# Performance work log

Measured on AMD Instinct MI355X. Metric: run time of the kernel, lower is better.

Reference implementation:

```python
import jax, jax.numpy as jnp
import numpy as np
from jax import lax

DN = ('NCHW', 'OIHW', 'NCHW')


def conv3x3(x, w, b):
    return lax.conv_general_dilated(x, w, (1, 1), 'SAME', dimension_numbers=DN) + b[None, :, None, None]


def conv1x1(x, w, b):
    # w: [O, I] -> pointwise conv
    return jnp.einsum('oi,bihw->bohw', w, x) + b[None, :, None, None]


def sft(x0, x1, sc0w, sc0b, sc1w, sc1b, sh0w, sh0b, sh1w, sh1b):
    scale = conv1x1(jax.nn.leaky_relu(conv1x1(x1, sc0w, sc0b), 0.1), sc1w, sc1b)
    shift = conv1x1(jax.nn.leaky_relu(conv1x1(x1, sh0w, sh0b), 0.1), sh1w, sh1b)
    return x0 * (scale + 1.0) + shift


def deform_conv(x, offset, w, b):
    # torchvision DeformConv2d, 3x3, stride 1, pad 1, dilation 1, no mask.
    B, C, H, W = x.shape
    O = w.shape[0]
    K = 9
    off = offset.reshape(B, K, 2, H, W)  # (dy, dx) per kernel tap
    ki = jnp.arange(3, dtype=x.dtype) - 1.0
    ky = jnp.repeat(ki, 3)  # [9]
    kx = jnp.tile(ki, 3)
    hh = jnp.arange(H, dtype=x.dtype)
    ww = jnp.arange(W, dtype=x.dtype)
    py = off[:, :, 0] + hh[None, None, :, None] + ky[None, :, None, None]  # [B,K,H,W]
    px = off[:, :, 1] + ww[None, None, None, :] + kx[None, :, None, None]
    y0f = jnp.floor(py)
    x0f = jnp.floor(px)
    wy = (py - y0f)[:, None]  # [B,1,K,H,W]
    wx = (px - x0f)[:, None]
    y0 = y0f.astype(jnp.int32)
    x0i = x0f.astype(jnp.int32)
    x_flat = x.reshape(B, C, H * W)

    def gather(iy, ix):
        valid = (iy >= 0) & (iy < H) & (ix >= 0) & (ix < W)
        idx = (jnp.clip(iy, 0, H - 1) * W + jnp.clip(ix, 0, W - 1)).reshape(B, K * H * W)
        vals = jax.vmap(lambda xf, ii: xf[:, ii])(x_flat, idx)  # [B,C,K*H*W]
        return vals.reshape(B, C, K, H, W) * valid[:, None].astype(x.dtype)

    v00 = gather(y0, x0i)
    v01 = gather(y0, x0i + 1)
    v10 = gather(y0 + 1, x0i)
    v11 = gather(y0 + 1, x0i + 1)
    samp = (v00 * (1 - wy) * (1 - wx) + v01 * (1 - wy) * wx
            + v10 * wy * (1 - wx) + v11 * wy * wx)  # [B,C,K,H,W]
    return jnp.einsum('bckhw,ock->bohw', samp, w.reshape(O, C, K)) + b[None, :, None, None]


def setup_inputs() -> dict:
    key = jax.random.key(0)
    ks = jax.random.split(key, 32)
    B, C0, C1, H, W = 4, 128, 32, 96, 96
    f32 = jnp.float32
    d = {
        'x0': jax.random.normal(ks[0], (B, C0, H, W), f32),
        'x1': jax.random.normal(ks[1], (B, C1, H, W), f32),
        'w_off': jax.random.normal(ks[2], (18, C0, 3, 3), f32) * 0.02,
        'b_off': jnp.zeros((18,), f32),
        's1_sc0_w': jax.random.normal(ks[3], (C0, C1), f32) * 0.05,
        's1_sc0_b': jnp.zeros((C0,), f32),
        's1_sc1_w': jax.random.normal(ks[4], (C0, C0), f32) * 0.05,
        's1_sc1_b': jnp.zeros((C0,), f32),
        's1_sh0_w': jax.random.normal(ks[5], (C0, C1), f32) * 0.05,
        's1_sh0_b': jnp.zeros((C0,), f32),
        's1_sh1_w': jax.random.normal(ks[6], (C0, C0), f32) * 0.05,
        's1_sh1_b': jnp.zeros((C0,), f32),
        'w_d1': jax.random.normal(ks[7], (C0, C0, 3, 3), f32) * 0.03,
        'b_d1': jnp.zeros((C0,), f32),
        's2_sc0_w': jax.random.normal(ks[8], (C0, C1), f32) * 0.05,
        's2_sc0_b': jnp.zeros((C0,), f32),
        's2_sc1_w': jax.random.normal(ks[9], (C0, C0), f32) * 0.05,
        's2_sc1_b': jnp.zeros((C0,), f32),
        's2_sh0_w': jax.random.normal(ks[10], (C0, C1), f32) * 0.05,
        's2_sh0_b': jnp.zeros((C0,), f32),
        's2_sh1_w': jax.random.normal(ks[11], (C0, C0), f32) * 0.05,
        's2_sh1_b': jnp.zeros((C0,), f32),
        'w_d2': jax.random.normal(ks[12], (C0, C0, 3, 3), f32) * 0.03,
        'b_d2': jnp.zeros((C0,), f32),
    }
    return d


def reference(x0, x1, w_off, b_off,
              s1_sc0_w, s1_sc0_b, s1_sc1_w, s1_sc1_b,
              s1_sh0_w, s1_sh0_b, s1_sh1_w, s1_sh1_b,
              w_d1, b_d1,
              s2_sc0_w, s2_sc0_b, s2_sc1_w, s2_sc1_b,
              s2_sh0_w, s2_sh0_b, s2_sh1_w, s2_sh1_b,
              w_d2, b_d2):
    off = conv3x3(x0, w_off, b_off)
    fea = sft(x0, x1, s1_sc0_w, s1_sc0_b, s1_sc1_w, s1_sc1_b,
              s1_sh0_w, s1_sh0_b, s1_sh1_w, s1_sh1_b)
    fea = jax.nn.relu(deform_conv(fea, off, w_d1, b_d1))
    fea = sft(fea, x1, s2_sc0_w, s2_sc0_b, s2_sc1_w, s2_sc1_b,
              s2_sh0_w, s2_sh0_b, s2_sh1_w, s2_sh1_b)
    fea = deform_conv(fea, off, w_d2, b_d2)
    return x0 + fea
```

## Files before the change

### kernel.cpp

```cpp
#include <hip/hip_runtime.h>

typedef unsigned short u16;
typedef unsigned int   u32;
typedef __attribute__((ext_vector_type(8))) _Float16 f16x8;
typedef __attribute__((ext_vector_type(2))) float f32x2;
typedef __attribute__((ext_vector_type(4))) float f32x4;
typedef __attribute__((ext_vector_type(16))) float f32x16;
typedef __attribute__((ext_vector_type(4))) unsigned int u32x4;

constexpr int B_  = 4;
constexpr int C0  = 128;
constexpr int C1  = 32;
constexpr int H_  = 96;
constexpr int W_  = 96;
constexpr int HW  = H_ * W_;
constexpr int PT  = 64;
constexpr int TPB = HW / PT;
constexpr int NTILE = B_ * TPB;

__device__ inline u16 f2h(float f) {
    _Float16 h = (_Float16)f;
    return __builtin_bit_cast(u16, h);
}

__global__ __launch_bounds__(256) void k_prep(
    const float* __restrict__ w_off,
    const float* __restrict__ wd1,  const float* __restrict__ wd2,
    const float* __restrict__ s1c0, const float* __restrict__ s1h0,
    const float* __restrict__ s2c0, const float* __restrict__ s2h0,
    const float* __restrict__ s1c1, const float* __restrict__ s1h1,
    const float* __restrict__ s2c1, const float* __restrict__ s2h1,
    float* __restrict__ wofft, u16* __restrict__ wdhi, u16* __restrict__ wdlo,
    u16* __restrict__ w0h,     u16* __restrict__ w1h)
{
    int t = blockIdx.x * 256 + threadIdx.x;
    if (t < C0 * 18 * 9) {
        int c = t / 162, r = t % 162, o = r / 9, tap = r % 9;
        wofft[t] = w_off[(o * C0 + c) * 9 + tap];
    }
    if (t < 2 * 9 * C0 * C0) {
        int d = t / (9 * C0 * C0), r = t % (9 * C0 * C0);
        int k = r / (C0 * C0), r2 = r % (C0 * C0), o = r2 / C0, c = r2 % C0;
        const float* wsrc = d ? wd2 : wd1;
        float wv = wsrc[(o * C0 + c) * 9 + k];
        _Float16 hi = (_Float16)wv;
        float rr = wv - (float)hi;
        wdhi[t] = __builtin_bit_cast(u16, hi);
        wdlo[t] = f2h(rr);
    }
    if (t < 4 * C0 * C1) {
        int m = t / (C0 * C1), i = t % (C0 * C1);
        const float* s = (m == 0) ? s1c0 : (m == 1) ? s1h0 : (m == 2) ? s2c0 : s2h0;
        w0h[t] = f2h(s[i]);
    }
    if (t < 4 * C0 * C0) {
        int m = t / (C0 * C0), i = t % (C0 * C0);
        const float* s = (m == 0) ? s1c1 : (m == 1) ? s1h1 : (m == 2) ? s2c1 : s2h1;
        w1h[t] = f2h(s[i]);
    }
}

__global__ __launch_bounds__(256) void k_conv_off(
    const float* __restrict__ x0, const float* __restrict__ wofft,
    const float* __restrict__ boff, float* __restrict__ off)
{
    int bx = blockIdx.x;
    int b  = bx / TPB;
    int p0 = (bx % TPB) * PT;
    int tid = threadIdx.x;
    int p   = tid & 63;
    int cq  = __builtin_amdgcn_readfirstlane(tid >> 6);
    int pos = p0 + p;
    int h = pos / W_, w = pos % W_;

    float acc[18];
#pragma unroll
    for (int o = 0; o < 18; ++o) acc[o] = 0.f;

    for (int cc = 0; cc < 32; ++cc) {
        int c = cq * 32 + cc;
        const float* xb = x0 + ((size_t)(b * C0 + c)) * HW;
        float v[9];
#pragma unroll
        for (int t = 0; t < 9; ++t) {
            int dy = t / 3 - 1, dx = t % 3 - 1;
            int hy = h + dy, wx = w + dx;
            bool ok = (hy >= 0) & (hy < H_) & (wx >= 0) & (wx < W_);
            v[t] = ok ? xb[hy * W_ + wx] : 0.f;
        }
        const float* wr = wofft + c * 162;
#pragma unroll
        for (int o = 0; o < 18; ++o)
#pragma unroll
            for (int t = 0; t < 9; ++t)
                acc[o] = fmaf(wr[o * 9 + t], v[t], acc[o]);
    }

    __shared__ float red[4][18][PT];
#pragma unroll
    for (int o = 0; o < 18; ++o) red[cq][o][p] = acc[o];
    __syncthreads();
    for (int idx = tid; idx < 18 * PT; idx += 256) {
        int o = idx / PT, pp = idx % PT;
        float s = red[0][o][pp] + red[1][o][pp] + red[2][o][pp] + red[3][o][pp]
                + boff[o];
        off[((size_t)(b * 18 + o)) * HW + p0 + pp] = s;
    }
}

template <int XSRC>
__global__ __launch_bounds__(512, 6) void k_sft_mma(
    const float* __restrict__ xf,
    const float* __restrict__ xT,
    const float* __restrict__ x1,
    const u16* __restrict__ w0s, const u16* __restrict__ w0h,
    const u16* __restrict__ w1s, const u16* __restrict__ w1h,
    const float* __restrict__ b0s, const float* __restrict__ b0h,
    const float* __restrict__ b1s, const float* __restrict__ b1h,
    float* __restrict__ outT)
{
    __shared__ __align__(16) u16 x1t[64 * 32];
    __shared__ __align__(16) u16 hidt[2][64 * 128];

    int bx = blockIdx.x, b = bx / TPB, p0 = (bx % TPB) * PT;
    int tid = threadIdx.x, l = tid & 63;
    int w = __builtin_amdgcn_readfirstlane(tid >> 6);
    f32x4 zz = {0.f, 0.f, 0.f, 0.f};

    for (int i = tid; i < C1 * PT; i += 512) {
        int ch = i >> 6, pos = i & 63;
        float v = x1[((size_t)(b * C1 + ch)) * HW + p0 + pos];
        x1t[pos * 32 + (ch ^ ((pos & 3) << 3))] = f2h(v);
    }
    __syncthreads();

    {
        int mt = w & 3, br = w >> 2;
        int pos = mt * 16 + (l & 15);
        int koff = (l >> 4) * 8;
        f16x8 a = *(const f16x8*)&x1t[pos * 32 + (koff ^ ((pos & 3) << 3))];
        const u16* w0 = br ? w0h : w0s;
        const float* bb = br ? b0h : b0s;
        u16* hrow = hidt[br];
#pragma unroll
        for (int nt = 0; nt < 8; ++nt) {
            int n = nt * 16 + (l & 15);
            f16x8 bfr = *(const f16x8*)&w0[n * 32 + koff];
            f32x4 h = __builtin_amdgcn_mfma_f32_16x16x32_f16(a, bfr, zz, 0, 0, 0);
            float bv = bb[n];
#pragma unroll
            for (int r = 0; r < 4; ++r) {
                float hv = h[r] + bv;
                hv = hv > 0.f ? hv : 0.1f * hv;
                int prow = mt * 16 + (l >> 4) * 4 + r;
                hrow[prow * 128 + (n ^ ((prow & 7) << 3))] = f2h(hv);
            }
        }
    }
    __syncthreads();

    f32x4 accS[4], accH[4];
#pragma unroll
    for (int nt = 0; nt < 4; ++nt) { accS[nt] = zz; accH[nt] = zz; }
    int mt = w & 3, nh = w >> 2;
    int pos = mt * 16 + (l & 15);
#pragma unroll
    for (int ks = 0; ks < 4; ++ks) {
        int kb = ks * 32 + (l >> 4) * 8;
        f16x8 aS = *(const f16x8*)&hidt[0][pos * 128 + (kb ^ ((pos & 7) << 3))];
        f16x8 aH = *(const f16x8*)&hidt[1][pos * 128 + (kb ^ ((pos & 7) << 3))];
#pragma unroll
        for (int nt = 0; nt < 4; ++nt) {
            int n = nh * 64 + nt * 16 + (l & 15);
            f16x8 bS = *(const f16x8*)&w1s[n * 128 + kb];
            f16x8 bH = *(const f16x8*)&w1h[n * 128 + kb];
            accS[nt] = __builtin_amdgcn_mfma_f32_16x16x32_f16(aS, bS, accS[nt], 0, 0, 0);
            accH[nt] = __builtin_amdgcn_mfma_f32_16x16x32_f16(aH, bH, accH[nt], 0, 0, 0);
        }
    }

#pragma unroll
    for (int nt = 0; nt < 4; ++nt) {
        int n = nh * 64 + nt * 16 + (l & 15);
        float scb = b1s[n], shb = b1h[n];
        float xv[4];
        if (XSRC == 0) {
            const float* xp = xf + ((size_t)(b * C0 + n)) * HW + p0 + mt * 16 + (l >> 4) * 4;
            f32x4 x4 = *(const f32x4*)xp;
#pragma unroll
            for (int r = 0; r < 4; ++r) xv[r] = x4[r];
        } else {
#pragma unroll
            for (int r = 0; r < 4; ++r)
                xv[r] = xT[((size_t)(b * HW + p0 + mt * 16 + (l >> 4) * 4 + r)) * C0 + n];
        }
#pragma unroll
        for (int r = 0; r < 4; ++r) {
            float scale = accS[nt][r] + scb + 1.f;
            float shift = accH[nt][r] + shb;
            outT[((size_t)(b * HW + p0 + mt * 16 + (l >> 4) * 4 + r)) * C0 + n]
                = xv[r] * scale + shift;
        }
    }
}

template <int MODE>
__global__ __launch_bounds__(512, 4) void k_deform10(
    const float* __restrict__ srcT,
    const float* __restrict__ off,
    const u16* __restrict__ whi,
    const u16* __restrict__ wlo,
    const float* __restrict__ bias,
    const float* __restrict__ x0,
    float* __restrict__ outF,
    float* __restrict__ outT)
{
    constexpr int SA = 136;
    constexpr int SB = 72;
    __shared__ __align__(16) u16   a_buf[2][64 * SA];
    __shared__ __align__(16) u16   b_buf[2][128 * SB];
    __shared__ __align__(16) u16   cidx[9 * 64 * 4];
    __shared__ __align__(16) float cwt[9 * 64 * 2];

    int bx = blockIdx.x;
    bx = (bx & 7) * (NTILE / 8) + (bx >> 3);
    int b = bx / TPB, p0 = (bx % TPB) * PT;
    int tid = threadIdx.x, l = tid & 63;
    int w = __builtin_amdgcn_readfirstlane(tid >> 6);
    int mh = w & 1, ng = w >> 1;
    int lr = l & 31, ksel = l >> 5;

    for (int e = tid; e < 9 * 64; e += 512) {
        int k = e >> 6, pp = e & 63;
        int pos = p0 + pp, h = pos / W_, wc = pos % W_;
        float dy = off[((size_t)(b * 18 + 2 * k)) * HW + pos];
        float dx = off[((size_t)(b * 18 + 2 * k + 1)) * HW + pos];
        float py = dy + (float)(h + k / 3 - 1);
        float px = dx + (float)(wc + k % 3 - 1);
        float yf = floorf(py), xf = floorf(px);
        int y0 = (int)yf, x0i = (int)xf;
        cwt[e * 2]     = py - yf;
        cwt[e * 2 + 1] = px - xf;
        int iy0 = min(max(y0, 0), H_ - 1),     iy1 = min(max(y0 + 1, 0), H_ - 1);
        int ix0 = min(max(x0i, 0), W_ - 1),    ix1 = min(max(x0i + 1, 0), W_ - 1);
        bool vy0 = (y0 >= 0) & (y0 < H_),      vy1 = (y0 + 1 >= 0) & (y0 + 1 < H_);
        bool vx0 = (x0i >= 0) & (x0i < W_),    vx1 = (x0i + 1 >= 0) & (x0i + 1 < W_);
        cidx[e * 4 + 0] = (u16)(iy0 * W_ + ix0) | ((vy0 & vx0) ? 0x8000 : 0);
        cidx[e * 4 + 1] = (u16)(iy0 * W_ + ix1) | ((vy0 & vx1) ? 0x8000 : 0);
        cidx[e * 4 + 2] = (u16)(iy1 * W_ + ix0) | ((vy1 & vx0) ? 0x8000 : 0);
        cidx[e * 4 + 3] = (u16)(iy1 * W_ + ix1) | ((vy1 & vx1) ? 0x8000 : 0);
    }
    __syncthreads();

    f32x16 acc;
#pragma unroll
    for (int i = 0; i < 16; ++i) acc[i] = 0.f;

    const float* lbase = srcT + (size_t)b * HW * C0 + 2 * l;
    int wrow = tid >> 2, wseg = tid & 3;

    f32x2 gv1[4][4], gv2[4][4];
    u32x4 wbh[2], wbl[2];

#define ISSUE_G(DST, KK, IOFF)                                                \
    {                                                                         \
        int ek = (KK) * 64 + w * 8 + (IOFF);                                  \
        _Pragma("unroll")                                                     \
        for (int i = 0; i < 4; ++i) {                                         \
            int e = ek + i;                                                   \
            u32 c01 = *(const u32*)&cidx[e * 4];                              \
            u32 c23 = *(const u32*)&cidx[e * 4 + 2];                          \
            DST[i][0] = *(const f32x2*)(lbase + (size_t)(c01 & 0x3fffu) * C0);\
            DST[i][1] = *(const f32x2*)(lbase + (size_t)((c01 >> 16) & 0x3fffu) * C0); \
            DST[i][2] = *(const f32x2*)(lbase + (size_t)(c23 & 0x3fffu) * C0);\
            DST[i][3] = *(const f32x2*)(lbase + (size_t)((c23 >> 16) & 0x3fffu) * C0); \
        }                                                                     \
    }

#define COMMIT_CH(SRC, KK, IOFF)                                              \
    {                                                                         \
        int ek = (KK) * 64 + w * 8 + (IOFF);                                  \
        _Pragma("unroll")                                                     \
        for (int i = 0; i < 4; ++i) {                                         \
            int e = ek + i, pp = w * 8 + (IOFF) + i;                          \
            u32 c01 = *(const u32*)&cidx[e * 4];                              \
            u32 c23 = *(const u32*)&cidx[e * 4 + 2];                          \
            float wy = cwt[e * 2], wx = cwt[e * 2 + 1];                       \
            float aa  = wy * wx;                                              \
            float w11 = (c23 & 0x80000000u) ? aa : 0.f;                       \
            float w10 = (c23 & 0x8000u) ? (wy - aa) : 0.f;                    \
            float w01 = (c01 & 0x80000000u) ? (wx - aa) : 0.f;                \
            float w00 = (c01 & 0x8000u) ? (1.f - wy - wx + aa) : 0.f;         \
            float s0 = SRC[i][0][0] * w00 + SRC[i][1][0] * w01                \
                     + SRC[i][2][0] * w10 + SRC[i][3][0] * w11;               \
            float s1 = SRC[i][0][1] * w00 + SRC[i][1][1] * w01                \
                     + SRC[i][2][1] * w10 + SRC[i][3][1] * w11;               \
            _Float16 h0 = (_Float16)s0, h1 = (_Float16)s1;                    \
            float r0 = s0 - (float)h0, r1 = s1 - (float)h1;                   \
            u32 hv = (u32)__builtin_bit_cast(u16, h0)                         \
                   | ((u32)__builtin_bit_cast(u16, h1) << 16);                \
            u32 lv = (u32)f2h(r0) | ((u32)f2h(r1) << 16);                     \
            *(u32*)&a_buf[0][pp * SA + 2 * l] = hv;                           \
            *(u32*)&a_buf[1][pp * SA + 2 * l] = lv;                           \
        }                                                                     \
    }

#define ISSUE_W(KK, KH)                                                       \
    {                                                                         \
        const u16* sh = whi + (size_t)(KK) * 16384 + wrow * 128 + (KH) * 64 + wseg * 16; \
        const u16* sl = wlo + (size_t)(KK) * 16384 + wrow * 128 + (KH) * 64 + wseg * 16; \
        wbh[0] = *(const u32x4*)&sh[0];  wbh[1] = *(const u32x4*)&sh[8];      \
        wbl[0] = *(const u32x4*)&sl[0];  wbl[1] = *(const u32x4*)&sl[8];      \
    }

#define WRITE_B()                                                             \
    {                                                                         \
        *(u32x4*)&b_buf[0][wrow * SB + wseg * 16]     = wbh[0];               \
        *(u32x4*)&b_buf[0][wrow * SB + wseg * 16 + 8] = wbh[1];               \
        *(u32x4*)&b_buf[1][wrow * SB + wseg * 16]     = wbl[0];               \
        *(u32x4*)&b_buf[1][wrow * SB + wseg * 16 + 8] = wbl[1];               \
    }

#define MFMA_PH(KH)                                                           \
    {                                                                         \
        _Pragma("unroll")                                                     \
        for (int ks = 0; ks < 4; ++ks) {                                      \
            int kA = (KH) * 64 + ks * 16 + ksel * 8;                          \
            int kB = ks * 16 + ksel * 8;                                      \
            f16x8 ah = *(const f16x8*)&a_buf[0][(mh * 32 + lr) * SA + kA];    \
            f16x8 al = *(const f16x8*)&a_buf[1][(mh * 32 + lr) * SA + kA];    \
            f16x8 bh = *(const f16x8*)&b_buf[0][(ng * 32 + lr) * SB + kB];    \
            f16x8 bl = *(const f16x8*)&b_buf[1][(ng * 32 + lr) * SB + kB];    \
            acc = __builtin_amdgcn_mfma_f32_32x32x16_f16(ah, bh, acc, 0, 0, 0); \
            acc = __builtin_amdgcn_mfma_f32_32x32x16_f16(al, bh, acc, 0, 0, 0); \
            acc = __builtin_amdgcn_mfma_f32_32x32x16_f16(ah, bl, acc, 0, 0, 0); \
        }                                                                     \
    }

#define LGKM_BAR                                                              \
    asm volatile("s_waitcnt lgkmcnt(0)" ::: "memory");                        \
    __builtin_amdgcn_s_barrier();

    ISSUE_G(gv1, 0, 0)
    ISSUE_G(gv2, 0, 4)
    ISSUE_W(0, 0)
    COMMIT_CH(gv1, 0, 0)
    COMMIT_CH(gv2, 0, 4)
    WRITE_B()
    ISSUE_W(0, 1)
    __builtin_amdgcn_sched_barrier(0);
    LGKM_BAR

    for (int k = 0; k < 9; ++k) {
        __builtin_amdgcn_s_setprio(1);
        MFMA_PH(0)
        __builtin_amdgcn_s_setprio(0);
        if (k < 8) ISSUE_G(gv1, k + 1, 0)
        __builtin_amdgcn_sched_barrier(0);
        LGKM_BAR
        WRITE_B()
        if (k < 8) { ISSUE_W(k + 1, 0) ISSUE_G(gv2, k + 1, 4) }
        __builtin_amdgcn_sched_barrier(0);
        LGKM_BAR
        __builtin_amdgcn_s_setprio(1);
        MFMA_PH(1)
        __builtin_amdgcn_s_setprio(0);
        LGKM_BAR
        if (k < 8) {
            COMMIT_CH(gv1, k + 1, 0)
            COMMIT_CH(gv2, k + 1, 4)
            WRITE_B()
            ISSUE_W(k + 1, 1)
        }
        __builtin_amdgcn_sched_barrier(0);
        LGKM_BAR
    }
#undef ISSUE_G
#undef COMMIT_CH
#undef ISSUE_W
#undef WRITE_B
#undef MFMA_PH
#undef LGKM_BAR

    int o = ng * 32 + lr;
    float bv = bias[o];
    if (MODE == 0) {
        __syncthreads();
        float* otile = (float*)&a_buf[0][0];
#pragma unroll
        for (int q = 0; q < 4; ++q) {
            int pr = mh * 32 + q * 8 + 4 * ksel;
#pragma unroll
            for (int r = 0; r < 4; ++r) {
                float v = acc[q * 4 + r] + bv;
                v = v > 0.f ? v : 0.f;
                otile[(pr + r) * 132 + o] = v;
            }
        }
        __syncthreads();
        float* dst = outT + ((size_t)(b * HW + p0)) * C0;
        for (int i = tid; i < 2048; i += 512) {
            int row = i >> 5, c = i & 31;
            *(f32x4*)&dst[row * 128 + c * 4] = *(const f32x4*)&otile[row * 132 + c * 4];
        }
    } else {
#pragma unroll
        for (int q = 0; q < 4; ++q) {
            int pr = mh * 32 + q * 8 + 4 * ksel;
            size_t base_o = ((size_t)(b * C0 + o)) * HW + p0 + pr;
            f32x4 x4 = *(const f32x4*)(x0 + base_o);
            f32x4 ov;
#pragma unroll
            for (int r = 0; r < 4; ++r) ov[r] = acc[q * 4 + r] + bv + x4[r];
            *(f32x4*)(outF + base_o) = ov;
        }
    }
}

constexpr size_t WB_OFF   = 0;
constexpr size_t WB_WOFFT = 2654208;
constexpr size_t WB_W0H   = 2737152;
constexpr size_t WB_W1H   = 2769920;
constexpr size_t WB_WDHI  = 2900992;
constexpr size_t WB_WDLO  = 4080640;
constexpr size_t WB_TA    = 5260288;
constexpr size_t WB_TB    = 24134656;

extern "C" void kernel_launch(void* const* d_in, const int* in_sizes, int n_in,
                              void* d_out, int out_size, void* d_ws, size_t ws_size,
                              hipStream_t stream)
{
    const float* x0      = (const float*)d_in[0];
    const float* x1      = (const float*)d_in[1];
    const float* w_off   = (const float*)d_in[2];
    const float* b_off   = (const float*)d_in[3];
    const float* s1_sc0w = (const float*)d_in[4];
    const float* s1_sc0b = (const float*)d_in[5];
    const float* s1_sc1w = (const float*)d_in[6];
    const float* s1_sc1b = (const float*)d_in[7];
    const float* s1_sh0w = (const float*)d_in[8];
    const float* s1_sh0b = (const float*)d_in[9];
    const float* s1_sh1w = (const float*)d_in[10];
    const float* s1_sh1b = (const float*)d_in[11];
    const float* w_d1    = (const float*)d_in[12];
    const float* b_d1    = (const float*)d_in[13];
    const float* s2_sc0w = (const float*)d_in[14];
    const float* s2_sc0b = (const float*)d_in[15];
    const float* s2_sc1w = (const float*)d_in[16];
    const float* s2_sc1b = (const float*)d_in[17];
    const float* s2_sh0w = (const float*)d_in[18];
    const float* s2_sh0b = (const float*)d_in[19];
    const float* s2_sh1w = (const float*)d_in[20];
    const float* s2_sh1b = (const float*)d_in[21];
    const float* w_d2    = (const float*)d_in[22];
    const float* b_d2    = (const float*)d_in[23];

    char* wsb = (char*)d_ws;
    float* off   = (float*)(wsb + WB_OFF);
    float* wofft = (float*)(wsb + WB_WOFFT);
    u16*   w0h   = (u16*)(wsb + WB_W0H);
    u16*   w1h   = (u16*)(wsb + WB_W1H);
    u16*   wdhi  = (u16*)(wsb + WB_WDHI);
    u16*   wdlo  = (u16*)(wsb + WB_WDLO);
    float* TA    = (float*)(wsb + WB_TA);
    float* TB    = (float*)(wsb + WB_TB);

    k_prep<<<1152, 256, 0, stream>>>(w_off, w_d1, w_d2,
                                     s1_sc0w, s1_sh0w, s2_sc0w, s2_sh0w,
                                     s1_sc1w, s1_sh1w, s2_sc1w, s2_sh1w,
                                     wofft, wdhi, wdlo, w0h, w1h);
    k_conv_off<<<NTILE, 256, 0, stream>>>(x0, wofft, b_off, off);
    k_sft_mma<0><<<NTILE, 512, 0, stream>>>(x0, nullptr, x1,
                                            w0h, w0h + 4096,
                                            w1h, w1h + 16384,
                                            s1_sc0b, s1_sh0b, s1_sc1b, s1_sh1b, TA);
    k_deform10<0><<<NTILE, 512, 0, stream>>>(TA, off, wdhi, wdlo, b_d1,
                                             nullptr, nullptr, TB);
    k_sft_mma<1><<<NTILE, 512, 0, stream>>>(nullptr, TB, x1,
                                            w0h + 8192, w0h + 12288,
                                            w1h + 32768, w1h + 49152,
                                            s2_sc0b, s2_sh0b, s2_sc1b, s2_sh1b, TA);
    k_deform10<1><<<NTILE, 512, 0, stream>>>(TA, off, wdhi + 9 * 16384, wdlo + 9 * 16384,
                                             b_d2, x0, (float*)d_out, nullptr);
}
```

Before: 376.8 us.

## Stream deform-conv weights straight to LDS with XOR-swizzled layout and single-buffer pipeline

```diff
diff --git a/kernel.cpp b/kernel.cpp
--- a/kernel.cpp
+++ b/kernel.cpp
@@ -30,7 +30,7 @@
     const float* __restrict__ s2c0, const float* __restrict__ s2h0,
     const float* __restrict__ s1c1, const float* __restrict__ s1h1,
     const float* __restrict__ s2c1, const float* __restrict__ s2h1,
-    float* __restrict__ wofft, u16* __restrict__ wdhi, u16* __restrict__ wdlo,
+    float* __restrict__ wofft, u16* __restrict__ wdsh, u16* __restrict__ wdsl,
     u16* __restrict__ w0h,     u16* __restrict__ w1h)
 {
     int t = blockIdx.x * 256 + threadIdx.x;
@@ -45,8 +45,11 @@
         float wv = wsrc[(o * C0 + c) * 9 + k];
         _Float16 hi = (_Float16)wv;
         float rr = wv - (float)hi;
-        wdhi[t] = __builtin_bit_cast(u16, hi);
-        wdlo[t] = f2h(rr);
+        int kh = c >> 6, cc = c & 63;
+        size_t dst = (((size_t)(d * 9 + k) * 2 + kh) * 8192)
+                   + o * 64 + (((cc & 56) ^ ((o & 7) << 3)) | (cc & 7));
+        wdsh[dst] = __builtin_bit_cast(u16, hi);
+        wdsl[dst] = f2h(rr);
     }
     if (t < 4 * C0 * C1) {
         int m = t / (C0 * C1), i = t % (C0 * C1);
@@ -205,22 +208,23 @@
 }
 
 template <int MODE>
-__global__ __launch_bounds__(512, 4) void k_deform10(
+__global__ __launch_bounds__(512, 4) void k_deform12(
     const float* __restrict__ srcT,
     const float* __restrict__ off,
-    const u16* __restrict__ whi,
-    const u16* __restrict__ wlo,
+    const u16* __restrict__ whiS,
+    const u16* __restrict__ wloS,
     const float* __restrict__ bias,
     const float* __restrict__ x0,
     float* __restrict__ outF,
     float* __restrict__ outT)
 {
-    constexpr int SA = 136;
-    constexpr int SB = 72;
-    __shared__ __align__(16) u16   a_buf[2][64 * SA];
-    __shared__ __align__(16) u16   b_buf[2][128 * SB];
-    __shared__ __align__(16) u16   cidx[9 * 64 * 4];
+    __shared__ __align__(16) u16   smem[16384 + 16384 + 2304];
     __shared__ __align__(16) float cwt[9 * 64 * 2];
+    u16* a_hi = smem;
+    u16* a_lo = smem + 8192;
+    u16* b_hi = smem + 16384;
+    u16* b_lo = smem + 16384 + 8192;
+    u16* cidx = smem + 32768;
 
     int bx = blockIdx.x;
     bx = (bx & 7) * (NTILE / 8) + (bx >> 3);
@@ -257,32 +261,46 @@
     for (int i = 0; i < 16; ++i) acc[i] = 0.f;
 
     const float* lbase = srcT + (size_t)b * HW * C0 + 2 * l;
-    int wrow = tid >> 2, wseg = tid & 3;
-
-    f32x2 gv1[4][4], gv2[4][4];
-    u32x4 wbh[2], wbl[2];
-
-#define ISSUE_G(DST, KK, IOFF)                                                \
+    f32x2 gv[8][4];
+
+#define GLOADB(KK, KH)                                                        \
     {                                                                         \
-        int ek = (KK) * 64 + w * 8 + (IOFF);                                  \
+        const u16* sh = whiS + (((size_t)(KK) * 2 + (KH)) * 8192);            \
+        const u16* sl = wloS + (((size_t)(KK) * 2 + (KH)) * 8192);            \
         _Pragma("unroll")                                                     \
-        for (int i = 0; i < 4; ++i) {                                         \
+        for (int i = 0; i < 2; ++i) {                                         \
+            __builtin_amdgcn_global_load_lds(                                 \
+                (const __attribute__((address_space(1))) unsigned int*)(sh + (tid + i * 512) * 8), \
+                (__attribute__((address_space(3))) unsigned int*)((char*)b_hi + ((tid & ~63) + i * 512) * 16), \
+                16, 0, 0);                                                    \
+            __builtin_amdgcn_global_load_lds(                                 \
+                (const __attribute__((address_space(1))) unsigned int*)(sl + (tid + i * 512) * 8), \
+                (__attribute__((address_space(3))) unsigned int*)((char*)b_lo + ((tid & ~63) + i * 512) * 16), \
+                16, 0, 0);                                                    \
+        }                                                                     \
+    }
+
+#define ISSUE_G(KK)                                                           \
+    {                                                                         \
+        int ek = (KK) * 64 + w * 8;                                           \
+        _Pragma("unroll")                                                     \
+        for (int i = 0; i < 8; ++i) {                                         \
             int e = ek + i;                                                   \
             u32 c01 = *(const u32*)&cidx[e * 4];                              \
             u32 c23 = *(const u32*)&cidx[e * 4 + 2];                          \
-            DST[i][0] = *(const f32x2*)(lbase + (size_t)(c01 & 0x3fffu) * C0);\
-            DST[i][1] = *(const f32x2*)(lbase + (size_t)((c01 >> 16) & 0x3fffu) * C0); \
-            DST[i][2] = *(const f32x2*)(lbase + (size_t)(c23 & 0x3fffu) * C0);\
-            DST[i][3] = *(const f32x2*)(lbase + (size_t)((c23 >> 16) & 0x3fffu) * C0); \
+            gv[i][0] = *(const f32x2*)(lbase + (size_t)(c01 & 0x3fffu) * C0); \
+            gv[i][1] = *(const f32x2*)(lbase + (size_t)((c01 >> 16) & 0x3fffu) * C0); \
+            gv[i][2] = *(const f32x2*)(lbase + (size_t)(c23 & 0x3fffu) * C0); \
+            gv[i][3] = *(const f32x2*)(lbase + (size_t)((c23 >> 16) & 0x3fffu) * C0); \
         }                                                                     \
     }
 
-#define COMMIT_CH(SRC, KK, IOFF)                                              \
+#define COMMIT_A(KK)                                                          \
     {                                                                         \
-        int ek = (KK) * 64 + w * 8 + (IOFF);                                  \
+        int ek = (KK) * 64 + w * 8;                                           \
         _Pragma("unroll")                                                     \
-        for (int i = 0; i < 4; ++i) {                                         \
-            int e = ek + i, pp = w * 8 + (IOFF) + i;                          \
+        for (int i = 0; i < 8; ++i) {                                         \
+            int e = ek + i, pp = w * 8 + i;                                   \
             u32 c01 = *(const u32*)&cidx[e * 4];                              \
             u32 c23 = *(const u32*)&cidx[e * 4 + 2];                          \
             float wy = cwt[e * 2], wx = cwt[e * 2 + 1];                       \
@@ -291,34 +309,19 @@
             float w10 = (c23 & 0x8000u) ? (wy - aa) : 0.f;                    \
             float w01 = (c01 & 0x80000000u) ? (wx - aa) : 0.f;                \
             float w00 = (c01 & 0x8000u) ? (1.f - wy - wx + aa) : 0.f;         \
-            float s0 = SRC[i][0][0] * w00 + SRC[i][1][0] * w01                \
-                     + SRC[i][2][0] * w10 + SRC[i][3][0] * w11;               \
-            float s1 = SRC[i][0][1] * w00 + SRC[i][1][1] * w01                \
-                     + SRC[i][2][1] * w10 + SRC[i][3][1] * w11;               \
+            float s0 = gv[i][0][0] * w00 + gv[i][1][0] * w01                  \
+                     + gv[i][2][0] * w10 + gv[i][3][0] * w11;                 \
+            float s1 = gv[i][0][1] * w00 + gv[i][1][1] * w01                  \
+                     + gv[i][2][1] * w10 + gv[i][3][1] * w11;                 \
             _Float16 h0 = (_Float16)s0, h1 = (_Float16)s1;                    \
             float r0 = s0 - (float)h0, r1 = s1 - (float)h1;                   \
             u32 hv = (u32)__builtin_bit_cast(u16, h0)                         \
                    | ((u32)__builtin_bit_cast(u16, h1) << 16);                \
             u32 lv = (u32)f2h(r0) | ((u32)f2h(r1) << 16);                     \
-            *(u32*)&a_buf[0][pp * SA + 2 * l] = hv;                           \
-            *(u32*)&a_buf[1][pp * SA + 2 * l] = lv;                           \
+            int ci = (2 * l) ^ ((pp & 7) << 3);                               \
+            *(u32*)&a_hi[pp * 128 + ci] = hv;                                 \
+            *(u32*)&a_lo[pp * 128 + ci] = lv;                                 \
         }                                                                     \
-    }
-
-#define ISSUE_W(KK, KH)                                                       \
-    {                                                                         \
-        const u16* sh = whi + (size_t)(KK) * 16384 + wrow * 128 + (KH) * 64 + wseg * 16; \
-        const u16* sl = wlo + (size_t)(KK) * 16384 + wrow * 128 + (KH) * 64 + wseg * 16; \
-        wbh[0] = *(const u32x4*)&sh[0];  wbh[1] = *(const u32x4*)&sh[8];      \
-        wbl[0] = *(const u32x4*)&sl[0];  wbl[1] = *(const u32x4*)&sl[8];      \
-    }
-
-#define WRITE_B()                                                             \
-    {                                                                         \
-        *(u32x4*)&b_buf[0][wrow * SB + wseg * 16]     = wbh[0];               \
-        *(u32x4*)&b_buf[0][wrow * SB + wseg * 16 + 8] = wbh[1];               \
-        *(u32x4*)&b_buf[1][wrow * SB + wseg * 16]     = wbl[0];               \
-        *(u32x4*)&b_buf[1][wrow * SB + wseg * 16 + 8] = wbl[1];               \
     }
 
 #define MFMA_PH(KH)                                                           \
@@ -327,66 +330,70 @@
         for (int ks = 0; ks < 4; ++ks) {                                      \
             int kA = (KH) * 64 + ks * 16 + ksel * 8;                          \
             int kB = ks * 16 + ksel * 8;                                      \
-            f16x8 ah = *(const f16x8*)&a_buf[0][(mh * 32 + lr) * SA + kA];    \
-            f16x8 al = *(const f16x8*)&a_buf[1][(mh * 32 + lr) * SA + kA];    \
-            f16x8 bh = *(const f16x8*)&b_buf[0][(ng * 32 + lr) * SB + kB];    \
-            f16x8 bl = *(const f16x8*)&b_buf[1][(ng * 32 + lr) * SB + kB];    \
+            int arow = mh * 32 + lr;                                          \
+            int au = arow * 128 + (kA ^ ((arow & 7) << 3));                   \
+            int brow = ng * 32 + lr;                                          \
+            int bu = brow * 64 + (kB ^ ((brow & 7) << 3));                    \
+            f16x8 ah = *(const f16x8*)&a_hi[au];                              \
+            f16x8 al = *(const f16x8*)&a_lo[au];                              \
+            f16x8 bh = *(const f16x8*)&b_hi[bu];                              \
+            f16x8 bl = *(const f16x8*)&b_lo[bu];                              \
             acc = __builtin_amdgcn_mfma_f32_32x32x16_f16(ah, bh, acc, 0, 0, 0); \
             acc = __builtin_amdgcn_mfma_f32_32x32x16_f16(al, bh, acc, 0, 0, 0); \
             acc = __builtin_amdgcn_mfma_f32_32x32x16_f16(ah, bl, acc, 0, 0, 0); \
         }                                                                     \
     }
 
-#define LGKM_BAR                                                              \
-    asm volatile("s_waitcnt lgkmcnt(0)" ::: "memory");                        \
-    __builtin_amdgcn_s_barrier();
-
-    ISSUE_G(gv1, 0, 0)
-    ISSUE_G(gv2, 0, 4)
-    ISSUE_W(0, 0)
-    COMMIT_CH(gv1, 0, 0)
-    COMMIT_CH(gv2, 0, 4)
-    WRITE_B()
-    ISSUE_W(0, 1)
-    __builtin_amdgcn_sched_barrier(0);
-    LGKM_BAR
-
-    for (int k = 0; k < 9; ++k) {
+#define BAR_LG   asm volatile("s_waitcnt lgkmcnt(0)" ::: "memory"); __builtin_amdgcn_s_barrier();
+#define BAR_LGV  asm volatile("s_waitcnt vmcnt(0) lgkmcnt(0)" ::: "memory"); __builtin_amdgcn_s_barrier();
+#define SB0      __builtin_amdgcn_sched_barrier(0);
+
+    GLOADB(0, 0) SB0
+    ISSUE_G(0) SB0
+    asm volatile("s_waitcnt vmcnt(0)" ::: "memory");
+    COMMIT_A(0)
+    BAR_LGV
+
+    for (int k = 0; k < 8; ++k) {
         __builtin_amdgcn_s_setprio(1);
         MFMA_PH(0)
         __builtin_amdgcn_s_setprio(0);
-        if (k < 8) ISSUE_G(gv1, k + 1, 0)
-        __builtin_amdgcn_sched_barrier(0);
-        LGKM_BAR
-        WRITE_B()
-        if (k < 8) { ISSUE_W(k + 1, 0) ISSUE_G(gv2, k + 1, 4) }
-        __builtin_amdgcn_sched_barrier(0);
-        LGKM_BAR
+        BAR_LG
+        GLOADB(k, 1) SB0
+        ISSUE_G(k + 1) SB0
+        asm volatile("s_waitcnt vmcnt(32)" ::: "memory");
+        __builtin_amdgcn_s_barrier();
         __builtin_amdgcn_s_setprio(1);
         MFMA_PH(1)
         __builtin_amdgcn_s_setprio(0);
-        LGKM_BAR
-        if (k < 8) {
-            COMMIT_CH(gv1, k + 1, 0)
-            COMMIT_CH(gv2, k + 1, 4)
-            WRITE_B()
-            ISSUE_W(k + 1, 1)
-        }
-        __builtin_amdgcn_sched_barrier(0);
-        LGKM_BAR
-    }
+        BAR_LG
+        GLOADB(k + 1, 0) SB0
+        COMMIT_A(k + 1)
+        BAR_LGV
+    }
+    __builtin_amdgcn_s_setprio(1);
+    MFMA_PH(0)
+    __builtin_amdgcn_s_setprio(0);
+    BAR_LG
+    GLOADB(8, 1) SB0
+    asm volatile("s_waitcnt vmcnt(0)" ::: "memory");
+    __builtin_amdgcn_s_barrier();
+    __builtin_amdgcn_s_setprio(1);
+    MFMA_PH(1)
+    __builtin_amdgcn_s_setprio(0);
+    BAR_LG
+#undef GLOADB
 #undef ISSUE_G
-#undef COMMIT_CH
-#undef ISSUE_W
-#undef WRITE_B
+#undef COMMIT_A
 #undef MFMA_PH
-#undef LGKM_BAR
+#undef BAR_LG
+#undef BAR_LGV
+#undef SB0
 
     int o = ng * 32 + lr;
     float bv = bias[o];
     if (MODE == 0) {
-        __syncthreads();
-        float* otile = (float*)&a_buf[0][0];
+        float* otile = (float*)smem;
 #pragma unroll
         for (int q = 0; q < 4; ++q) {
             int pr = mh * 32 + q * 8 + 4 * ksel;
@@ -421,10 +428,10 @@
 constexpr size_t WB_WOFFT = 2654208;
 constexpr size_t WB_W0H   = 2737152;
 constexpr size_t WB_W1H   = 2769920;
-constexpr size_t WB_WDHI  = 2900992;
-constexpr size_t WB_WDLO  = 4080640;
-constexpr size_t WB_TA    = 5260288;
-constexpr size_t WB_TB    = 24134656;
+constexpr size_t WB_WDSH  = 2900992;
+constexpr size_t WB_WDSL  = 3490816;
+constexpr size_t WB_TA    = 4080640;
+constexpr size_t WB_TB    = 22955008;
 
 extern "C" void kernel_launch(void* const* d_in, const int* in_sizes, int n_in,
                               void* d_out, int out_size, void* d_ws, size_t ws_size,
@@ -460,26 +467,26 @@
     float* wofft = (float*)(wsb + WB_WOFFT);
     u16*   w0h   = (u16*)(wsb + WB_W0H);
     u16*   w1h   = (u16*)(wsb + WB_W1H);
-    u16*   wdhi  = (u16*)(wsb + WB_WDHI);
-    u16*   wdlo  = (u16*)(wsb + WB_WDLO);
+    u16*   wdsh  = (u16*)(wsb + WB_WDSH);
+    u16*   wdsl  = (u16*)(wsb + WB_WDSL);
     float* TA    = (float*)(wsb + WB_TA);
     float* TB    = (float*)(wsb + WB_TB);
 
     k_prep<<<1152, 256, 0, stream>>>(w_off, w_d1, w_d2,
                                      s1_sc0w, s1_sh0w, s2_sc0w, s2_sh0w,
                                      s1_sc1w, s1_sh1w, s2_sc1w, s2_sh1w,
-                                     wofft, wdhi, wdlo, w0h, w1h);
+                                     wofft, wdsh, wdsl, w0h, w1h);
     k_conv_off<<<NTILE, 256, 0, stream>>>(x0, wofft, b_off, off);
     k_sft_mma<0><<<NTILE, 512, 0, stream>>>(x0, nullptr, x1,
                                             w0h, w0h + 4096,
                                             w1h, w1h + 16384,
                                             s1_sc0b, s1_sh0b, s1_sc1b, s1_sh1b, TA);
-    k_deform10<0><<<NTILE, 512, 0, stream>>>(TA, off, wdhi, wdlo, b_d1,
+    k_deform12<0><<<NTILE, 512, 0, stream>>>(TA, off, wdsh, wdsl, b_d1,
                                              nullptr, nullptr, TB);
     k_sft_mma<1><<<NTILE, 512, 0, stream>>>(nullptr, TB, x1,
                                             w0h + 8192, w0h + 12288,
                                             w1h + 32768, w1h + 49152,
                                             s2_sc0b, s2_sh0b, s2_sc1b, s2_sh1b, TA);
-    k_deform10<1><<<NTILE, 512, 0, stream>>>(TA, off, wdhi + 9 * 16384, wdlo + 9 * 16384,
+    k_deform12<1><<<NTILE, 512, 0, stream>>>(TA, off, wdsh + 9 * 16384, wdsl + 9 * 16384,
                                              b_d2, x0, (float*)d_out, nullptr);
 }
```

Result: no change. 378.9 us (+0.6%).
